# Performance work log

Measured on AMD Instinct MI355X. Metric: run time of the kernel, lower is better.

## Reference

```python
import jax, jax.numpy as jnp
import numpy as np

B_BATCH = 128
IN_F = 1024
OUT_F = 1024
CODE = 2
FACTOR = 1.0


def setup_inputs() -> dict:
    key = jax.random.key(0)
    k = jax.random.split(key, 7)
    bound = 1.0 / np.sqrt(IN_F)
    return {
        "input": jax.random.normal(k[0], (B_BATCH, IN_F), dtype=jnp.float32),
        "codes": jax.random.normal(k[1], (B_BATCH, CODE, CODE), dtype=jnp.float32),
        "weight": jax.random.uniform(k[2], (IN_F, OUT_F), minval=-bound, maxval=bound, dtype=jnp.float32),
        "A": jax.random.uniform(k[3], (IN_F, CODE), minval=-bound, maxval=bound, dtype=jnp.float32),
        "B": jax.random.uniform(k[4], (CODE, OUT_F), minval=-bound, maxval=bound, dtype=jnp.float32),
        "bias": jax.random.uniform(k[5], (OUT_F,), minval=-bound, maxval=bound, dtype=jnp.float32),
        "bias_context": jax.random.uniform(k[6], (CODE, OUT_F), minval=-bound, maxval=bound, dtype=jnp.float32),
    }


def reference(input, codes, weight, A, B, bias, bias_context):
    # per-sample low-rank modulation: A [in,code] x codes [b,code,code] -> [b,in,code]
    w = jnp.einsum('ir,brp->bip', A, codes)
    # [b,in,code] x B [code,out] -> [b,in,out]
    context_weights = jnp.einsum('bir,rj->bij', w, B)
    # diag(codes) [b,code] @ bias_context [code,out] -> [b,out]
    context_bias = jnp.diagonal(codes, axis1=-2, axis2=-1) @ bias_context
    combined_weight = weight + FACTOR * context_weights  # [b,in,out]
    combined_bias = bias + FACTOR * context_bias          # [b,out]
    return jnp.einsum('bi,bij->bj', input, combined_weight) + combined_bias
```

## Files before the change

kernel.cpp:

```cpp
#include <hip/hip_runtime.h>

#define N_BATCH 128
#define IN_F 1024
#define OUT_F 1024
#define J4 (OUT_F / 4)

template <int CHUNK>
__global__ __launch_bounds__(256) void gemm_partial(
    const float* __restrict__ input,
    const float* __restrict__ weight,
    float* __restrict__ ws)
{
    __shared__ float s_in[2][CHUNK];
    const int t = threadIdx.x;
    const int bBase = blockIdx.x * 2;
    const int kIdx = blockIdx.y;
    const int i0 = kIdx * CHUNK;

    {
        const int n4 = CHUNK / 4;
        #pragma unroll
        for (int r = 0; r < 2; ++r) {
            const float4* src = (const float4*)(input + (size_t)(bBase + r) * IN_F + i0);
            float4* dst = (float4*)&s_in[r][0];
            for (int x = t; x < n4; x += 256) dst[x] = src[x];
        }
    }
    __syncthreads();

    const float4* wp = (const float4*)weight + (size_t)i0 * J4 + t;
    float4 acc0 = {0.f, 0.f, 0.f, 0.f};
    float4 acc1 = {0.f, 0.f, 0.f, 0.f};

    #pragma unroll 8
    for (int ii = 0; ii < CHUNK; ++ii) {
        const float4 w = wp[(size_t)ii * J4];
        const float a0 = s_in[0][ii];
        const float a1 = s_in[1][ii];
        acc0.x = fmaf(a0, w.x, acc0.x);
        acc0.y = fmaf(a0, w.y, acc0.y);
        acc0.z = fmaf(a0, w.z, acc0.z);
        acc0.w = fmaf(a0, w.w, acc0.w);
        acc1.x = fmaf(a1, w.x, acc1.x);
        acc1.y = fmaf(a1, w.y, acc1.y);
        acc1.z = fmaf(a1, w.z, acc1.z);
        acc1.w = fmaf(a1, w.w, acc1.w);
    }

    float4* wsp = (float4*)ws;
    const size_t base = ((size_t)kIdx * N_BATCH + bBase) * J4 + t;
    wsp[base] = acc0;
    wsp[base + J4] = acc1;
}

__global__ __launch_bounds__(256) void reduce_epilogue(
    const float* __restrict__ input,
    const float* __restrict__ codes,
    const float* __restrict__ A,
    const float* __restrict__ Bm,
    const float* __restrict__ bias,
    const float* __restrict__ bctx,
    const float* __restrict__ ws,
    float* __restrict__ out,
    int kc)
{
    const int b = blockIdx.x;
    const int t = threadIdx.x;

    float p0 = 0.f, p1 = 0.f;
    for (int i = t; i < IN_F; i += 256) {
        const float x = input[(size_t)b * IN_F + i];
        p0 = fmaf(x, A[i * 2 + 0], p0);
        p1 = fmaf(x, A[i * 2 + 1], p1);
    }
    #pragma unroll
    for (int off = 32; off > 0; off >>= 1) {
        p0 += __shfl_down(p0, off, 64);
        p1 += __shfl_down(p1, off, 64);
    }
    __shared__ float s_part[4][2];
    __shared__ float s_v[4];
    const int wave = t >> 6;
    if ((t & 63) == 0) { s_part[wave][0] = p0; s_part[wave][1] = p1; }
    __syncthreads();
    if (t == 0) {
        const float u0 = s_part[0][0] + s_part[1][0] + s_part[2][0] + s_part[3][0];
        const float u1 = s_part[0][1] + s_part[1][1] + s_part[2][1] + s_part[3][1];
        const float c00 = codes[b * 4 + 0], c01 = codes[b * 4 + 1];
        const float c10 = codes[b * 4 + 2], c11 = codes[b * 4 + 3];
        s_v[0] = fmaf(u0, c00, u1 * c10);
        s_v[1] = fmaf(u0, c01, u1 * c11);
        s_v[2] = c00;
        s_v[3] = c11;
    }
    __syncthreads();
    const float v0 = s_v[0], v1 = s_v[1], c00 = s_v[2], c11 = s_v[3];

    const float4* wsp = (const float4*)ws;
    float4 sum = {0.f, 0.f, 0.f, 0.f};
    for (int k = 0; k < kc; ++k) {
        const float4 p = wsp[((size_t)k * N_BATCH + b) * J4 + t];
        sum.x += p.x; sum.y += p.y; sum.z += p.z; sum.w += p.w;
    }
    const float4 B0 = ((const float4*)Bm)[t];
    const float4 B1 = ((const float4*)Bm)[J4 + t];
    const float4 bi = ((const float4*)bias)[t];
    const float4 bc0 = ((const float4*)bctx)[t];
    const float4 bc1 = ((const float4*)bctx)[J4 + t];

    float4 r;
    r.x = sum.x + v0 * B0.x + v1 * B1.x + bi.x + c00 * bc0.x + c11 * bc1.x;
    r.y = sum.y + v0 * B0.y + v1 * B1.y + bi.y + c00 * bc0.y + c11 * bc1.y;
    r.z = sum.z + v0 * B0.z + v1 * B1.z + bi.z + c00 * bc0.z + c11 * bc1.z;
    r.w = sum.w + v0 * B0.w + v1 * B1.w + bi.w + c00 * bc0.w + c11 * bc1.w;
    ((float4*)out)[(size_t)b * J4 + t] = r;
}

extern "C" void kernel_launch(void* const* d_in, const int* in_sizes, int n_in,
                              void* d_out, int out_size, void* d_ws, size_t ws_size,
                              hipStream_t stream) {
    const float* input = (const float*)d_in[0];
    const float* codes = (const float*)d_in[1];
    const float* weight = (const float*)d_in[2];
    const float* A = (const float*)d_in[3];
    const float* Bm = (const float*)d_in[4];
    const float* bias = (const float*)d_in[5];
    const float* bctx = (const float*)d_in[6];
    float* out = (float*)d_out;
    float* ws = (float*)d_ws;

    const size_t per_chunk = (size_t)N_BATCH * OUT_F * sizeof(float);
    int kc;
    if (ws_size >= 8 * per_chunk)      kc = 8;
    else if (ws_size >= 4 * per_chunk) kc = 4;
    else if (ws_size >= 2 * per_chunk) kc = 2;
    else                               kc = 1;

    dim3 block(256);
    dim3 grid1(N_BATCH / 2, kc);
    switch (kc) {
        case 8: gemm_partial<128><<<grid1, block, 0, stream>>>(input, weight, ws); break;
        case 4: gemm_partial<256><<<grid1, block, 0, stream>>>(input, weight, ws); break;
        case 2: gemm_partial<512><<<grid1, block, 0, stream>>>(input, weight, ws); break;
        default: gemm_partial<1024><<<grid1, block, 0, stream>>>(input, weight, ws); break;
    }
    reduce_epilogue<<<dim3(N_BATCH), block, 0, stream>>>(
        input, codes, A, Bm, bias, bctx, ws, out, kc);
}
```

Measured before the change: 85.39 us.

## Retile split-K GEMM to 16 batch rows per block with 16 K-chunks

```diff
diff --git a/kernel.cpp b/kernel.cpp
--- a/kernel.cpp
+++ b/kernel.cpp
@@ -3,54 +3,48 @@
 #define N_BATCH 128
 #define IN_F 1024
 #define OUT_F 1024
-#define J4 (OUT_F / 4)
+#define KC 16
+#define CHUNK (IN_F / KC)
+#define BT 16
 
-template <int CHUNK>
 __global__ __launch_bounds__(256) void gemm_partial(
     const float* __restrict__ input,
     const float* __restrict__ weight,
     float* __restrict__ ws)
 {
-    __shared__ float s_in[2][CHUNK];
+    __shared__ float s_in[BT][CHUNK];
     const int t = threadIdx.x;
-    const int bBase = blockIdx.x * 2;
-    const int kIdx = blockIdx.y;
-    const int i0 = kIdx * CHUNK;
+    const int jBase = blockIdx.x * 256;
+    const int b0 = blockIdx.y * BT;
+    const int k = blockIdx.z;
+    const int i0 = k * CHUNK;
 
     {
-        const int n4 = CHUNK / 4;
-        #pragma unroll
-        for (int r = 0; r < 2; ++r) {
-            const float4* src = (const float4*)(input + (size_t)(bBase + r) * IN_F + i0);
-            float4* dst = (float4*)&s_in[r][0];
-            for (int x = t; x < n4; x += 256) dst[x] = src[x];
-        }
+        const int row = t >> 4;
+        const int x = t & 15;
+        ((float4*)&s_in[row][0])[x] =
+            ((const float4*)(input + (size_t)(b0 + row) * IN_F + i0))[x];
     }
     __syncthreads();
 
-    const float4* wp = (const float4*)weight + (size_t)i0 * J4 + t;
-    float4 acc0 = {0.f, 0.f, 0.f, 0.f};
-    float4 acc1 = {0.f, 0.f, 0.f, 0.f};
+    const int j = jBase + t;
+    const float* wp = weight + (size_t)i0 * OUT_F + j;
+    float acc[BT];
+    #pragma unroll
+    for (int r = 0; r < BT; ++r) acc[r] = 0.f;
 
-    #pragma unroll 8
+    #pragma unroll 4
     for (int ii = 0; ii < CHUNK; ++ii) {
-        const float4 w = wp[(size_t)ii * J4];
-        const float a0 = s_in[0][ii];
-        const float a1 = s_in[1][ii];
-        acc0.x = fmaf(a0, w.x, acc0.x);
-        acc0.y = fmaf(a0, w.y, acc0.y);
-        acc0.z = fmaf(a0, w.z, acc0.z);
-        acc0.w = fmaf(a0, w.w, acc0.w);
-        acc1.x = fmaf(a1, w.x, acc1.x);
-        acc1.y = fmaf(a1, w.y, acc1.y);
-        acc1.z = fmaf(a1, w.z, acc1.z);
-        acc1.w = fmaf(a1, w.w, acc1.w);
+        const float w = wp[(size_t)ii * OUT_F];
+        #pragma unroll
+        for (int r = 0; r < BT; ++r)
+            acc[r] = fmaf(s_in[r][ii], w, acc[r]);
     }
 
-    float4* wsp = (float4*)ws;
-    const size_t base = ((size_t)kIdx * N_BATCH + bBase) * J4 + t;
-    wsp[base] = acc0;
-    wsp[base + J4] = acc1;
+    float* o = ws + ((size_t)k * N_BATCH + b0) * OUT_F + j;
+    #pragma unroll
+    for (int r = 0; r < BT; ++r)
+        o[(size_t)r * OUT_F] = acc[r];
 }
 
 __global__ __launch_bounds__(256) void reduce_epilogue(
@@ -61,22 +55,24 @@
     const float* __restrict__ bias,
     const float* __restrict__ bctx,
     const float* __restrict__ ws,
-    float* __restrict__ out,
-    int kc)
+    float* __restrict__ out)
 {
-    const int b = blockIdx.x;
     const int t = threadIdx.x;
+    const int b = blockIdx.y;
+    const int j = blockIdx.x * 256 + t;
 
     float p0 = 0.f, p1 = 0.f;
-    for (int i = t; i < IN_F; i += 256) {
+    #pragma unroll
+    for (int ii = 0; ii < IN_F / 256; ++ii) {
+        const int i = t + 256 * ii;
         const float x = input[(size_t)b * IN_F + i];
         p0 = fmaf(x, A[i * 2 + 0], p0);
         p1 = fmaf(x, A[i * 2 + 1], p1);
     }
     #pragma unroll
     for (int off = 32; off > 0; off >>= 1) {
-        p0 += __shfl_down(p0, off, 64);
-        p1 += __shfl_down(p1, off, 64);
+        p0 += __shfl_down(p0, off);
+        p1 += __shfl_down(p1, off);
     }
     __shared__ float s_part[4][2];
     __shared__ float s_v[4];
@@ -96,24 +92,16 @@
     __syncthreads();
     const float v0 = s_v[0], v1 = s_v[1], c00 = s_v[2], c11 = s_v[3];
 
-    const float4* wsp = (const float4*)ws;
-    float4 sum = {0.f, 0.f, 0.f, 0.f};
-    for (int k = 0; k < kc; ++k) {
-        const float4 p = wsp[((size_t)k * N_BATCH + b) * J4 + t];
-        sum.x += p.x; sum.y += p.y; sum.z += p.z; sum.w += p.w;
-    }
-    const float4 B0 = ((const float4*)Bm)[t];
-    const float4 B1 = ((const float4*)Bm)[J4 + t];
-    const float4 bi = ((const float4*)bias)[t];
-    const float4 bc0 = ((const float4*)bctx)[t];
-    const float4 bc1 = ((const float4*)bctx)[J4 + t];
+    float sum = 0.f;
+    #pragma unroll
+    for (int k = 0; k < KC; ++k)
+        sum += ws[((size_t)k * N_BATCH + b) * OUT_F + j];
 
-    float4 r;
-    r.x = sum.x + v0 * B0.x + v1 * B1.x + bi.x + c00 * bc0.x + c11 * bc1.x;
-    r.y = sum.y + v0 * B0.y + v1 * B1.y + bi.y + c00 * bc0.y + c11 * bc1.y;
-    r.z = sum.z + v0 * B0.z + v1 * B1.z + bi.z + c00 * bc0.z + c11 * bc1.z;
-    r.w = sum.w + v0 * B0.w + v1 * B1.w + bi.w + c00 * bc0.w + c11 * bc1.w;
-    ((float4*)out)[(size_t)b * J4 + t] = r;
+    const float r = sum
+                  + v0 * Bm[j] + v1 * Bm[OUT_F + j]
+                  + bias[j]
+                  + c00 * bctx[j] + c11 * bctx[OUT_F + j];
+    out[(size_t)b * OUT_F + j] = r;
 }
 
 extern "C" void kernel_launch(void* const* d_in, const int* in_sizes, int n_in,
@@ -129,21 +117,11 @@
     float* out = (float*)d_out;
     float* ws = (float*)d_ws;
 
-    const size_t per_chunk = (size_t)N_BATCH * OUT_F * sizeof(float);
-    int kc;
-    if (ws_size >= 8 * per_chunk)      kc = 8;
-    else if (ws_size >= 4 * per_chunk) kc = 4;
-    else if (ws_size >= 2 * per_chunk) kc = 2;
-    else                               kc = 1;
+    dim3 block(256);
+    dim3 grid1(OUT_F / 256, N_BATCH / BT, KC);
+    gemm_partial<<<grid1, block, 0, stream>>>(input, weight, ws);
 
-    dim3 block(256);
-    dim3 grid1(N_BATCH / 2, kc);
-    switch (kc) {
-        case 8: gemm_partial<128><<<grid1, block, 0, stream>>>(input, weight, ws); break;
-        case 4: gemm_partial<256><<<grid1, block, 0, stream>>>(input, weight, ws); break;
-        case 2: gemm_partial<512><<<grid1, block, 0, stream>>>(input, weight, ws); break;
-        default: gemm_partial<1024><<<grid1, block, 0, stream>>>(input, weight, ws); break;
-    }
-    reduce_epilogue<<<dim3(N_BATCH), block, 0, stream>>>(
-        input, codes, A, Bm, bias, bctx, ws, out, kc);
+    dim3 grid2(OUT_F / 256, N_BATCH);
+    reduce_epilogue<<<grid2, block, 0, stream>>>(
+        input, codes, A, Bm, bias, bctx, ws, out);
 }
```

Measured after the change: 83.36 us. 2.4% less time.
